# Kernel tuning notes

Measured on AMD Instinct MI355X. Metric: run time of the kernel, lower is better.

The kernel has to match this reference:

```python
import jax, jax.numpy as jnp
import numpy as np

N_HEADS = 4
TAU = 0.1

def _ln(x, w, b):
    m = jnp.mean(x, axis=-1, keepdims=True)
    v = jnp.mean(jnp.square(x - m), axis=-1, keepdims=True)
    return (x - m) / jnp.sqrt(v + 1e-6) * w + b

def _l2norm(x):
    # torch F.normalize(dim=1): x / max(||x||_2, 1e-12)
    n = jnp.linalg.norm(x, axis=1, keepdims=True)
    return x / jnp.maximum(n, 1e-12)

def _sincos_pe(T, dim):
    pos = jnp.arange(T, dtype=jnp.float32)[:, None]
    div = jnp.exp(jnp.arange(0, dim, 2, dtype=jnp.float32) * (-np.log(10000.0) / dim))
    ang = pos * div[None, :]
    # interleave: even indices sin, odd indices cos
    return jnp.stack([jnp.sin(ang), jnp.cos(ang)], axis=-1).reshape(T, dim)

def reference(x, p1_w, p1_b, pln1_w, pln1_b, p2_w, pln2_w, pln2_b,
              in_proj_w, in_proj_b, out_proj_w, out_proj_b,
              ln1_w, ln1_b, lin1_w, lin1_b, lin2_w, lin2_b, ln2_w, ln2_b, head_w):
    B, T, D = x.shape
    E = p2_w.shape[0]           # bottleneck_dim = 256
    H = N_HEADS
    hd = E // H
    # projector: Linear -> LN -> GELU -> Linear(no bias) -> LN
    h = jax.nn.gelu(_ln(x.reshape(B * T, D) @ p1_w.T + p1_b, pln1_w, pln1_b), approximate=False)
    h = _ln(h @ p2_w.T, pln2_w, pln2_b).reshape(B, T, E)
    h = h + _sincos_pe(T, E)[None]
    causal = jnp.tril(jnp.ones((T, T), dtype=bool))
    L = in_proj_w.shape[0]
    for i in range(L):  # post-norm TransformerEncoderLayer
        qkv = h @ in_proj_w[i].T + in_proj_b[i]        # [B,T,3E]
        q, k, v = jnp.split(qkv, 3, axis=-1)
        q = q.reshape(B, T, H, hd).transpose(0, 2, 1, 3)
        k = k.reshape(B, T, H, hd).transpose(0, 2, 1, 3)
        v = v.reshape(B, T, H, hd).transpose(0, 2, 1, 3)
        scores = jnp.einsum('bhtd,bhsd->bhts', q, k) / np.float32(np.sqrt(hd))
        scores = jnp.where(causal[None, None], scores, -jnp.inf)
        probs = jax.nn.softmax(scores, axis=-1)        # materialized attn probs (eager path)
        attn = jnp.einsum('bhts,bhsd->bhtd', probs, v).transpose(0, 2, 1, 3).reshape(B, T, E)
        attn = attn @ out_proj_w[i].T + out_proj_b[i]
        h = _ln(h + attn, ln1_w[i], ln1_b[i])
        ff = jax.nn.gelu(h @ lin1_w[i].T + lin1_b[i], approximate=False) @ lin2_w[i].T + lin2_b[i]
        h = _ln(h + ff, ln2_w[i], ln2_b[i])
    flat = _l2norm(h.reshape(B * T, E))
    wn = _l2norm(head_w)
    return (flat @ wn.T / TAU).reshape(B, T, -1)

def setup_inputs() -> dict:
    key = jax.random.key(0)
    ks = jax.random.split(key, 8)
    B, T, D, E, HID, CLS, L = 2048, 20, 2048, 256, 1024, 1000, 2
    s = 0.02
    def w(k, shape):
        return jax.random.normal(k, shape, jnp.float32) * s
    return {
        'x': jax.random.normal(ks[0], (B, T, D), jnp.float32),
        'p1_w': w(ks[1], (HID, D)), 'p1_b': jnp.zeros((HID,), jnp.float32),
        'pln1_w': jnp.ones((HID,), jnp.float32), 'pln1_b': jnp.zeros((HID,), jnp.float32),
        'p2_w': w(ks[2], (E, HID)),
        'pln2_w': jnp.ones((E,), jnp.float32), 'pln2_b': jnp.zeros((E,), jnp.float32),
        'in_proj_w': w(ks[3], (L, 3 * E, E)), 'in_proj_b': jnp.zeros((L, 3 * E), jnp.float32),
        'out_proj_w': w(ks[4], (L, E, E)), 'out_proj_b': jnp.zeros((L, E), jnp.float32),
        'ln1_w': jnp.ones((L, E), jnp.float32), 'ln1_b': jnp.zeros((L, E), jnp.float32),
        'lin1_w': w(ks[5], (L, 4 * E, E)), 'lin1_b': jnp.zeros((L, 4 * E), jnp.float32),
        'lin2_w': w(ks[6], (L, E, 4 * E)), 'lin2_b': jnp.zeros((L, E), jnp.float32),
        'ln2_w': jnp.ones((L, E), jnp.float32), 'ln2_b': jnp.zeros((L, E), jnp.float32),
        'head_w': w(ks[7], (CLS, E)),
    }
```

## Files before the change

### kernel.cpp

```cpp
#include <hip/hip_runtime.h>
#include <math.h>

#define CDIV(a,b) (((a)+(b)-1)/(b))

typedef unsigned short bfu;
typedef short   s16x8 __attribute__((ext_vector_type(8)));
typedef float   f32x4 __attribute__((ext_vector_type(4)));

#define GLOAD16(gp, lp) __builtin_amdgcn_global_load_lds( \
    (const __attribute__((address_space(1))) void*)(gp),  \
    (__attribute__((address_space(3))) void*)(lp), 16, 0, 0)

static __device__ __forceinline__ float gelu_exact(float x) {
    return 0.5f * x * (1.0f + erff(x * 0.7071067811865475f));
}
static __device__ __forceinline__ bfu f2bf(float x) {
    unsigned int u = __float_as_uint(x);
    unsigned int r = u + 0x7fffu + ((u >> 16) & 1u);
    return (bfu)(r >> 16);
}
static __device__ __forceinline__ float bf2f(bfu b) {
    return __uint_as_float(((unsigned int)b) << 16);
}
static __device__ __forceinline__ float wave_sum(float v) {
    #pragma unroll
    for (int off = 32; off; off >>= 1) v += __shfl_xor(v, off, 64);
    return v;
}

__global__ __launch_bounds__(256)
void cvt_kernel(const float* __restrict__ in, bfu* __restrict__ out, int n4)
{
    int i = blockIdx.x * 256 + threadIdx.x;
    const int stride = gridDim.x * 256;
    for (; i < n4; i += stride) {
        float4 f = ((const float4*)in)[i];
        ushort4 o;
        o.x = f2bf(f.x); o.y = f2bf(f.y); o.z = f2bf(f.z); o.w = f2bf(f.w);
        ((ushort4*)out)[i] = o;
    }
}

__global__ __launch_bounds__(256)
void cvt6_kernel(const float* __restrict__ s0, const float* __restrict__ s1,
                 const float* __restrict__ s2, const float* __restrict__ s3,
                 const float* __restrict__ s4, const float* __restrict__ s5,
                 bfu* __restrict__ dst)
{
    const int c0 = 524288;
    const int c1 = c0 + 65536;
    const int c2 = c1 + 98304;
    const int c3 = c2 + 32768;
    const int c4 = c3 + 131072;
    const int c5 = c4 + 131072;
    int i = blockIdx.x * 256 + threadIdx.x;
    const int stride = gridDim.x * 256;
    for (; i < c5; i += stride) {
        const float* s; int base;
        if      (i < c0) { s = s0; base = 0;  }
        else if (i < c1) { s = s1; base = c0; }
        else if (i < c2) { s = s2; base = c1; }
        else if (i < c3) { s = s3; base = c2; }
        else if (i < c4) { s = s4; base = c3; }
        else             { s = s5; base = c4; }
        float4 f = ((const float4*)s)[i - base];
        ushort4 o;
        o.x = f2bf(f.x); o.y = f2bf(f.y); o.z = f2bf(f.z); o.w = f2bf(f.w);
        ((ushort4*)dst)[i] = o;
    }
}

__global__ __launch_bounds__(256)
void pe_kernel(float* __restrict__ pe)
{
    const int t = blockIdx.x;
    const int c = threadIdx.x;
    const float div = expf((float)(c & ~1) * (-9.210340371976184f / 256.0f));
    const float ang = (float)t * div;
    pe[t * 256 + c] = (c & 1) ? cosf(ang) : sinf(ang);
}

template<bool GELU_EP, bool OUT_BF16>
__global__ __launch_bounds__(512, 4)
void mfma_gemmA(const bfu* __restrict__ A, const bfu* __restrict__ W,
                const float* __restrict__ bias, void* __restrict__ Cv,
                int M, int N, int K, float scale, int ntx)
{
    __shared__ bfu ldsA[3][4096];
    __shared__ bfu ldsW[3][8192];

    const int tid  = threadIdx.x;
    const int lane = tid & 63;
    const int wv   = tid >> 6;
    const int nwg  = gridDim.x;
    const int lid  = (nwg & 7) ? (int)blockIdx.x
                               : ((int)blockIdx.x & 7) * (nwg >> 3) + ((int)blockIdx.x >> 3);
    const int row0 = (lid / ntx) * 128;
    const int col0 = (lid % ntx) * 256;

    const int srow = wv * 16 + (lane >> 2);
    const int sk   = ((lane & 3) ^ ((lane >> 2) & 3) ^ (lane >> 4)) * 8;
    const bfu* aS  = A + (size_t)(row0 + srow) * K + sk;
    const bfu* wS0 = W + (size_t)(col0 + srow)        * K + sk;
    const bfu* wS1 = W + (size_t)(col0 + srow + 128)  * K + sk;
    const int dOff = wv * 512;

    const int wr = wv >> 2, wc = wv & 3;
    const int fr = lane & 15;
    const int g4 = lane >> 4;
    const int slot = ((g4 ^ (fr & 3) ^ ((fr >> 2) & 3))) * 8;

    f32x4 acc[4][4];
    #pragma unroll
    for (int i = 0; i < 4; ++i)
        #pragma unroll
        for (int j = 0; j < 4; ++j) acc[i][j] = (f32x4)0.f;

    const int nt = K >> 5;

#define STAGEA_(b_, t_) do { \
    const size_t ko_ = (size_t)(t_) * 32; \
    GLOAD16(aS  + ko_, &ldsA[b_][dOff]); \
    GLOAD16(wS0 + ko_, &ldsW[b_][dOff]); \
    GLOAD16(wS1 + ko_, &ldsW[b_][4096 + dOff]); \
} while (0)

    STAGEA_(0, 0);
    STAGEA_(1, 1);

    int cur = 0, nxt2 = 2;
    for (int t = 0; t < nt; ++t) {
        if (t + 1 < nt) asm volatile("s_waitcnt vmcnt(3)" ::: "memory");
        else            asm volatile("s_waitcnt vmcnt(0)" ::: "memory");
        asm volatile("s_barrier" ::: "memory");

        if (t + 2 < nt) STAGEA_(nxt2, t + 2);

        const bfu* Ab = ldsA[cur];
        const bfu* Wb = ldsW[cur];

        s16x8 bfr[4], afr[4];
        #pragma unroll
        for (int j = 0; j < 4; ++j)
            bfr[j] = *(const s16x8*)&Wb[(wc * 64 + j * 16 + fr) * 32 + slot];
        #pragma unroll
        for (int i = 0; i < 4; ++i)
            afr[i] = *(const s16x8*)&Ab[(wr * 64 + i * 16 + fr) * 32 + slot];

        __builtin_amdgcn_s_setprio(1);
        #pragma unroll
        for (int i = 0; i < 4; ++i)
            #pragma unroll
            for (int j = 0; j < 4; ++j)
                acc[i][j] = __builtin_amdgcn_mfma_f32_16x16x32_bf16(afr[i], bfr[j], acc[i][j], 0, 0, 0);
        __builtin_amdgcn_s_setprio(0);

        cur  = (cur  == 2) ? 0 : cur  + 1;
        nxt2 = (nxt2 == 2) ? 0 : nxt2 + 1;
    }
#undef STAGEA_

    #pragma unroll
    for (int i = 0; i < 4; ++i) {
        const int r = row0 + wr * 64 + 16 * i + g4 * 4;
        #pragma unroll
        for (int j = 0; j < 4; ++j) {
            const int c = col0 + wc * 64 + 16 * j + fr;
            if (c < N) {
                const float bsum = bias ? bias[c] : 0.f;
                #pragma unroll
                for (int rr = 0; rr < 4; ++rr) {
                    float v = acc[i][j][rr] + bsum;
                    if (GELU_EP) v = gelu_exact(v);
                    v *= scale;
                    if (OUT_BF16) ((bfu*)Cv)[(size_t)(r + rr) * N + c] = f2bf(v);
                    else          ((float*)Cv)[(size_t)(r + rr) * N + c] = v;
                }
            }
        }
    }
}

template<bool RES, bool ADD_PE, bool L2N>
__global__ __launch_bounds__(512, 2)
void mfma_gemm_ln(const bfu* __restrict__ A, const bfu* __restrict__ W,
                  const float* __restrict__ bias, const float* __restrict__ R,
                  const float* __restrict__ lnw, const float* __restrict__ lnb,
                  const float* __restrict__ pe, float* __restrict__ Yf,
                  bfu* __restrict__ Yb, int M, int K, int T)
{
    __shared__ bfu ldsA[3][4096];
    __shared__ bfu ldsW[3][8192];

    const int tid  = threadIdx.x;
    const int lane = tid & 63;
    const int wv   = tid >> 6;
    const int nwg  = gridDim.x;
    const int lid  = (nwg & 7) ? (int)blockIdx.x
                               : ((int)blockIdx.x & 7) * (nwg >> 3) + ((int)blockIdx.x >> 3);
    const int row0 = lid * 128;

    const int srow = wv * 16 + (lane >> 2);
    const int sk   = ((lane & 3) ^ ((lane >> 2) & 3) ^ (lane >> 4)) * 8;
    const bfu* aS  = A + (size_t)(row0 + srow) * K + sk;
    const bfu* wS0 = W + (size_t)(srow)        * K + sk;
    const bfu* wS1 = W + (size_t)(srow + 128)  * K + sk;
    const int dOff = wv * 512;

    const int wr = wv >> 2, wc = wv & 3;
    const int fr = lane & 15;
    const int g4 = lane >> 4;
    const int slot = ((g4 ^ (fr & 3) ^ ((fr >> 2) & 3))) * 8;

    f32x4 acc[4][4];
    #pragma unroll
    for (int i = 0; i < 4; ++i)
        #pragma unroll
        for (int j = 0; j < 4; ++j) acc[i][j] = (f32x4)0.f;

    const int nt = K >> 5;

#define STAGELN(b_, t_) do { \
    const size_t ko_ = (size_t)(t_) * 32; \
    GLOAD16(aS  + ko_, &ldsA[b_][dOff]); \
    GLOAD16(wS0 + ko_, &ldsW[b_][dOff]); \
    GLOAD16(wS1 + ko_, &ldsW[b_][4096 + dOff]); \
} while (0)

    STAGELN(0, 0);
    STAGELN(1, 1);

    int cur = 0, nxt2 = 2;
    for (int t = 0; t < nt; ++t) {
        if (t + 1 < nt) asm volatile("s_waitcnt vmcnt(3)" ::: "memory");
        else            asm volatile("s_waitcnt vmcnt(0)" ::: "memory");
        asm volatile("s_barrier" ::: "memory");

        if (t + 2 < nt) STAGELN(nxt2, t + 2);

        const bfu* Ab = ldsA[cur];
        const bfu* Wb = ldsW[cur];

        s16x8 bfr[4], afr[4];
        #pragma unroll
        for (int j = 0; j < 4; ++j)
            bfr[j] = *(const s16x8*)&Wb[(wc * 64 + j * 16 + fr) * 32 + slot];
        #pragma unroll
        for (int i = 0; i < 4; ++i)
            afr[i] = *(const s16x8*)&Ab[(wr * 64 + i * 16 + fr) * 32 + slot];

        __builtin_amdgcn_s_setprio(1);
        #pragma unroll
        for (int i = 0; i < 4; ++i)
            #pragma unroll
            for (int j = 0; j < 4; ++j)
                acc[i][j] = __builtin_amdgcn_mfma_f32_16x16x32_bf16(afr[i], bfr[j], acc[i][j], 0, 0, 0);
        __builtin_amdgcn_s_setprio(0);

        cur  = (cur  == 2) ? 0 : cur  + 1;
        nxt2 = (nxt2 == 2) ? 0 : nxt2 + 1;
    }
#undef STAGELN

    __syncthreads();

    float* red   = (float*)ldsA;
    float* stats = red + 1024;

    float bj[4];
    #pragma unroll
    for (int j = 0; j < 4; ++j)
        bj[j] = bias ? bias[wc * 64 + j * 16 + fr] : 0.f;

    #pragma unroll
    for (int i = 0; i < 4; ++i) {
        #pragma unroll
        for (int rr = 0; rr < 4; ++rr) {
            const int rl = wr * 64 + i * 16 + g4 * 4 + rr;
            const size_t r = (size_t)(row0 + rl);
            float s = 0.f, q = 0.f;
            #pragma unroll
            for (int j = 0; j < 4; ++j) {
                float v = acc[i][j][rr] + bj[j];
                if (RES) v += R[r * 256 + (wc * 64 + j * 16 + fr)];
                acc[i][j][rr] = v;
                s += v; q += v * v;
            }
            #pragma unroll
            for (int off = 1; off < 16; off <<= 1) {
                s += __shfl_xor(s, off, 64);
                q += __shfl_xor(q, off, 64);
            }
            if (fr == 0) { red[rl * 4 + wc] = s; red[512 + rl * 4 + wc] = q; }
        }
    }
    __syncthreads();
    if (tid < 128) {
        const float s = red[tid*4+0] + red[tid*4+1] + red[tid*4+2] + red[tid*4+3];
        const float q = red[512+tid*4+0] + red[512+tid*4+1] + red[512+tid*4+2] + red[512+tid*4+3];
        const float mean = s * (1.f / 256.f);
        const float var  = q * (1.f / 256.f) - mean * mean;
        stats[tid]       = mean;
        stats[128 + tid] = rsqrtf(var + 1e-6f);
    }
    __syncthreads();

    float lw[4], lb[4];
    #pragma unroll
    for (int j = 0; j < 4; ++j) {
        const int c = wc * 64 + j * 16 + fr;
        lw[j] = lnw[c]; lb[j] = lnb[c];
    }
    #pragma unroll
    for (int i = 0; i < 4; ++i) {
        #pragma unroll
        for (int rr = 0; rr < 4; ++rr) {
            const int rl = wr * 64 + i * 16 + g4 * 4 + rr;
            const size_t r = (size_t)(row0 + rl);
            const float mean = stats[rl], rstd = stats[128 + rl];
            const int tmod = (int)(r % (size_t)T);
            float ysq = 0.f;
            #pragma unroll
            for (int j = 0; j < 4; ++j) {
                const int c = wc * 64 + j * 16 + fr;
                float y = (acc[i][j][rr] - mean) * rstd * lw[j] + lb[j];
                if (ADD_PE) y += pe[tmod * 256 + c];
                if (!L2N) {
                    Yf[r * 256 + c] = y;
                    Yb[r * 256 + c] = f2bf(y);
                } else {
                    acc[i][j][rr] = y;
                    ysq += y * y;
                }
            }
            if (L2N) {
                #pragma unroll
                for (int off = 1; off < 16; off <<= 1) ysq += __shfl_xor(ysq, off, 64);
                if (fr == 0) red[rl * 4 + wc] = ysq;
            }
        }
    }
    if (L2N) {
        __syncthreads();
        if (tid < 128) {
            const float n = sqrtf(red[tid*4+0] + red[tid*4+1] + red[tid*4+2] + red[tid*4+3]);
            stats[tid] = 1.f / fmaxf(n, 1e-12f);
        }
        __syncthreads();
        #pragma unroll
        for (int i = 0; i < 4; ++i) {
            #pragma unroll
            for (int rr = 0; rr < 4; ++rr) {
                const int rl = wr * 64 + i * 16 + g4 * 4 + rr;
                const size_t r = (size_t)(row0 + rl);
                const float rn = stats[rl];
                #pragma unroll
                for (int j = 0; j < 4; ++j) {
                    const int c = wc * 64 + j * 16 + fr;
                    Yb[r * 256 + c] = f2bf(acc[i][j][rr] * rn);
                }
            }
        }
    }
}

__global__ __launch_bounds__(256)
void ln1024_kernel(const bfu* __restrict__ X, const float* __restrict__ w,
                   const float* __restrict__ b, bfu* __restrict__ Y)
{
    __shared__ float sbuf[4];
    const int row = blockIdx.x;
    const bfu* xr = X + (size_t)row * 1024;

    ushort4 t4 = *(const ushort4*)(xr + threadIdx.x * 4);
    float v[4] = {bf2f(t4.x), bf2f(t4.y), bf2f(t4.z), bf2f(t4.w)};

    float s = v[0] + v[1] + v[2] + v[3];
    s = wave_sum(s);
    const int lane = threadIdx.x & 63, wid = threadIdx.x >> 6;
    if (lane == 0) sbuf[wid] = s;
    __syncthreads();
    const float mean = (sbuf[0] + sbuf[1] + sbuf[2] + sbuf[3]) * (1.f / 1024.f);

    float q = 0.f;
    #pragma unroll
    for (int j = 0; j < 4; ++j) { float d = v[j] - mean; q += d * d; }
    q = wave_sum(q);
    __syncthreads();
    if (lane == 0) sbuf[wid] = q;
    __syncthreads();
    const float var  = (sbuf[0] + sbuf[1] + sbuf[2] + sbuf[3]) * (1.f / 1024.f);
    const float rstd = rsqrtf(var + 1e-6f);

    ushort4 o;
    #pragma unroll
    for (int j = 0; j < 4; ++j) {
        const int c = threadIdx.x * 4 + j;
        float y = gelu_exact((v[j] - mean) * rstd * w[c] + b[c]);
        ((bfu*)&o)[j] = f2bf(y);
    }
    *(ushort4*)(Y + (size_t)row * 1024 + threadIdx.x * 4) = o;
}

__global__ __launch_bounds__(64)
void attn_kernel(const bfu* __restrict__ qkv, bfu* __restrict__ out,
                 int B, int T, int H)
{
    __shared__ float qs[20][65];
    __shared__ float ks[20][65];
    __shared__ float vs[20][65];
    __shared__ float probs[64];

    const int blk = blockIdx.x;
    const int b = blk / H;
    const int h = blk % H;
    const int tid = threadIdx.x;

    const bfu* base0 = qkv + (size_t)(b * T) * 768 + h * 64;
    #pragma unroll
    for (int m = 0; m < 3; ++m) {
        const bfu* src = base0 + m * 256;
        float (*dst)[65] = (m == 0) ? qs : (m == 1) ? ks : vs;
        #pragma unroll
        for (int i = 0; i < 5; ++i) {
            const int idx = i * 64 + tid;
            const int t = idx >> 4, s = (idx & 15) * 4;
            ushort4 u = *(const ushort4*)(src + (size_t)t * 768 + s);
            dst[t][s+0] = bf2f(u.x); dst[t][s+1] = bf2f(u.y);
            dst[t][s+2] = bf2f(u.z); dst[t][s+3] = bf2f(u.w);
        }
    }
    __syncthreads();

    for (int t = 0; t < T; ++t) {
        float sc = -INFINITY;
        if (tid <= t) {
            float s = 0.f;
            #pragma unroll
            for (int d = 0; d < 64; ++d) s = fmaf(qs[t][d], ks[tid][d], s);
            sc = s * 0.125f;
        }
        float m = sc;
        #pragma unroll
        for (int off = 32; off; off >>= 1) m = fmaxf(m, __shfl_xor(m, off, 64));
        float p = (tid <= t) ? expf(sc - m) : 0.f;
        float sum = p;
        #pragma unroll
        for (int off = 32; off; off >>= 1) sum += __shfl_xor(sum, off, 64);
        p /= sum;
        probs[tid] = p;
        __syncthreads();

        float o = 0.f;
        for (int s = 0; s <= t; ++s) o = fmaf(probs[s], vs[s][tid], o);
        out[(size_t)(b * T + t) * 256 + h * 64 + tid] = f2bf(o);
        __syncthreads();
    }
}

__global__ __launch_bounds__(256)
void l2norm_kernel(const float* __restrict__ X, bfu* __restrict__ Y)
{
    const int row  = blockIdx.x * 4 + (threadIdx.x >> 6);
    const int lane = threadIdx.x & 63;
    float4 v = *(const float4*)(X + (size_t)row * 256 + lane * 4);
    float n = sqrtf(wave_sum(v.x*v.x + v.y*v.y + v.z*v.z + v.w*v.w));
    n = 1.f / fmaxf(n, 1e-12f);
    ushort4 o = {f2bf(v.x*n), f2bf(v.y*n), f2bf(v.z*n), f2bf(v.w*n)};
    *(ushort4*)(Y + (size_t)row * 256 + lane * 4) = o;
}

extern "C" void kernel_launch(void* const* d_in, const int* in_sizes, int n_in,
                              void* d_out, int out_size, void* d_ws, size_t ws_size,
                              hipStream_t stream)
{
    const float* x         = (const float*)d_in[0];
    const float* p1_w      = (const float*)d_in[1];
    const float* p1_b      = (const float*)d_in[2];
    const float* pln1_w    = (const float*)d_in[3];
    const float* pln1_b    = (const float*)d_in[4];
    const float* p2_w      = (const float*)d_in[5];
    const float* pln2_w    = (const float*)d_in[6];
    const float* pln2_b    = (const float*)d_in[7];
    const float* in_proj_w = (const float*)d_in[8];
    const float* in_proj_b = (const float*)d_in[9];
    const float* out_proj_w= (const float*)d_in[10];
    const float* out_proj_b= (const float*)d_in[11];
    const float* ln1_w     = (const float*)d_in[12];
    const float* ln1_b     = (const float*)d_in[13];
    const float* lin1_w    = (const float*)d_in[14];
    const float* lin1_b    = (const float*)d_in[15];
    const float* lin2_w    = (const float*)d_in[16];
    const float* lin2_b    = (const float*)d_in[17];
    const float* ln2_w     = (const float*)d_in[18];
    const float* ln2_b     = (const float*)d_in[19];
    const float* head_w    = (const float*)d_in[20];

    const int B = 2048, T = 20, E = 256, HID = 1024, CLS = 1000, L = 2, H = 4;
    const int M = B * T;
    const int D = 2048;

    char* p = (char*)d_ws;
    bfu*   xb     = (bfu*)p;    p += (size_t)M * D * 2;
    bfu*   h1b    = (bfu*)p;    p += (size_t)M * HID * 2;
    bfu*   wblk   = (bfu*)p;    p += (size_t)3932160 * 2;
    bfu*   wnb    = (bfu*)p;    p += (size_t)1024 * E * 2;
    float* pe     = (float*)p;  p += (size_t)T * 256 * 4;

    char* q = (char*)xb;
    float* h      = (float*)q;  q += (size_t)M * E * 4;
    bfu*   hb     = (bfu*)q;    q += (size_t)M * E * 2;
    bfu*   abf    = (bfu*)q;    q += (size_t)M * E * 2;

    bfu* p1wb  = wblk;
    bfu* p2wb  = p1wb  + (size_t)HID * D;
    bfu* qkvwb = p2wb  + (size_t)E * HID;
    bfu* outwb = qkvwb + (size_t)L * 3 * E * E;
    bfu* l1wb  = outwb + (size_t)L * E * E;
    bfu* l2wb  = l1wb  + (size_t)L * 4 * E * E;

    float* out   = (float*)d_out;
    bfu*   qkvb  = (bfu*)d_out;

    cvt_kernel<<<2048, 256, 0, stream>>>(x, xb, M * D / 4);
    cvt6_kernel<<<2048, 256, 0, stream>>>(p1_w, p2_w, in_proj_w, out_proj_w, lin1_w, lin2_w, wblk);
    pe_kernel<<<T, 256, 0, stream>>>(pe);

    mfma_gemmA<false, true><<<dim3((M/128) * (HID/256)), 512, 0, stream>>>(
        xb, p1wb, p1_b, h1b, M, HID, D, 1.f, HID/256);
    ln1024_kernel<<<M, 256, 0, stream>>>(h1b, pln1_w, pln1_b, h1b);
    mfma_gemm_ln<false, true, false><<<dim3(M/128), 512, 0, stream>>>(
        h1b, p2wb, nullptr, nullptr, pln2_w, pln2_b, pe, h, hb, M, HID, T);

    for (int l = 0; l < L; ++l) {
        mfma_gemmA<false, true><<<dim3((M/128) * 3), 512, 0, stream>>>(
            hb, qkvwb + (size_t)l * 3*E*E, in_proj_b + (size_t)l * 3*E, qkvb, M, 3*E, E, 1.f, 3);
        attn_kernel<<<B * H, 64, 0, stream>>>(qkvb, abf, B, T, H);
        mfma_gemm_ln<true, false, false><<<dim3(M/128), 512, 0, stream>>>(
            abf, outwb + (size_t)l * E*E, out_proj_b + (size_t)l * E, h,
            ln1_w + (size_t)l * E, ln1_b + (size_t)l * E, nullptr, h, hb, M, E, T);
        mfma_gemmA<true, true><<<dim3((M/128) * 4), 512, 0, stream>>>(
            hb, l1wb + (size_t)l * 4*E*E, lin1_b + (size_t)l * 4*E, h1b, M, HID, E, 1.f, 4);
        if (l < L - 1) {
            mfma_gemm_ln<true, false, false><<<dim3(M/128), 512, 0, stream>>>(
                h1b, l2wb + (size_t)l * E*4*E, lin2_b + (size_t)l * E, h,
                ln2_w + (size_t)l * E, ln2_b + (size_t)l * E, nullptr, h, hb, M, HID, T);
        } else {
            mfma_gemm_ln<true, false, true><<<dim3(M/128), 512, 0, stream>>>(
                h1b, l2wb + (size_t)l * E*4*E, lin2_b + (size_t)l * E, h,
                ln2_w + (size_t)l * E, ln2_b + (size_t)l * E, nullptr, nullptr, hb, M, HID, T);
        }
    }

    l2norm_kernel<<<CLS/4, 256, 0, stream>>>(head_w, wnb);
    mfma_gemmA<false, false><<<dim3((M/128) * 4), 512, 0, stream>>>(
        hb, wnb, nullptr, out, M, CLS, E, 10.f, 4);
}
```

Baseline: 1.184 ms.

## Add 256x256-tile ping-pong MFMA GEMM for the first projector layer

Adds a new bf16 MFMA GEMM kernel with 256x256 output tiles, a double-buffered LDS pipeline split into two K-halves, and interleaved barriers with s_setprio around MFMA bursts. It replaces the 128x256-tile kernel for the large x @ p1_w GEMM (K=2048). The goal is more reuse per LDS load and better overlap of global loads with MFMA work. In exchange it uses more registers and LDS per block, which lowers occupancy to two blocks per CU and halves the grid size.

```diff
diff --git a/kernel.cpp b/kernel.cpp
--- a/kernel.cpp
+++ b/kernel.cpp
@@ -78,6 +78,145 @@
     const float div = expf((float)(c & ~1) * (-9.210340371976184f / 256.0f));
     const float ang = (float)t * div;
     pe[t * 256 + c] = (c & 1) ? cosf(ang) : sinf(ang);
+}
+
+template<bool OUT_BF16>
+__global__ __launch_bounds__(512, 2)
+void mfma_gemm8p(const bfu* __restrict__ A, const bfu* __restrict__ W,
+                 const float* __restrict__ bias, void* __restrict__ Cv,
+                 int M, int N, int K, float scale, int ntx)
+{
+    __shared__ bfu ldsA[2][2][8192];
+    __shared__ bfu ldsB[2][2][8192];
+
+    const int tid  = threadIdx.x;
+    const int lane = tid & 63;
+    const int wv   = tid >> 6;
+    const int nwg  = gridDim.x;
+    const int lid  = (nwg & 7) ? (int)blockIdx.x
+                               : ((int)blockIdx.x & 7) * (nwg >> 3) + ((int)blockIdx.x >> 3);
+    const int row0 = (lid / ntx) * 256;
+    const int col0 = (lid % ntx) * 256;
+
+    const int srow = wv * 16 + (lane >> 2);
+    const int sk   = ((lane & 3) ^ ((lane >> 2) & 3) ^ (lane >> 4)) * 8;
+    const bfu* aR0 = A + (size_t)(row0 + srow)       * K + sk;
+    const bfu* aR1 = A + (size_t)(row0 + 128 + srow) * K + sk;
+    const bfu* wR0 = W + (size_t)(col0 + srow)       * K + sk;
+    const bfu* wR1 = W + (size_t)(col0 + 128 + srow) * K + sk;
+    const int dOff = wv * 512;
+
+    const int wr = wv >> 2, wc = wv & 3;
+    const int fr = lane & 15;
+    const int g4 = lane >> 4;
+    const int slot = ((g4 ^ (fr & 3) ^ ((fr >> 2) & 3))) * 8;
+
+    f32x4 acc[8][4];
+    #pragma unroll
+    for (int i = 0; i < 8; ++i)
+        #pragma unroll
+        for (int j = 0; j < 4; ++j) acc[i][j] = (f32x4)0.f;
+
+    const int nt = K >> 6;
+
+#define STG8(t_, kh_) do { \
+    const size_t ko_ = (size_t)(t_) * 64 + (size_t)(kh_) * 32; \
+    const int b_ = (t_) & 1; \
+    GLOAD16(aR0 + ko_, &ldsA[b_][kh_][dOff]); \
+    GLOAD16(aR1 + ko_, &ldsA[b_][kh_][4096 + dOff]); \
+    GLOAD16(wR0 + ko_, &ldsB[b_][kh_][dOff]); \
+    GLOAD16(wR1 + ko_, &ldsB[b_][kh_][4096 + dOff]); \
+} while (0)
+
+    STG8(0, 0); STG8(0, 1); STG8(1, 0); STG8(1, 1);
+
+    for (int t = 0; t < nt; ++t) {
+        const int buf = t & 1;
+        if (t + 1 < nt) asm volatile("s_waitcnt vmcnt(8)" ::: "memory");
+        else            asm volatile("s_waitcnt vmcnt(0)" ::: "memory");
+        __builtin_amdgcn_s_barrier();
+
+        const bfu* Ab0 = ldsA[buf][0];
+        const bfu* Bb0 = ldsB[buf][0];
+        const bfu* Ab1 = ldsA[buf][1];
+        const bfu* Bb1 = ldsB[buf][1];
+
+        s16x8 a[8], b[4];
+        #pragma unroll
+        for (int mi = 0; mi < 8; ++mi)
+            a[mi] = *(const s16x8*)&Ab0[(wr * 128 + mi * 16 + fr) * 32 + slot];
+        b[0] = *(const s16x8*)&Bb0[(wc * 64 +  0 + fr) * 32 + slot];
+        b[1] = *(const s16x8*)&Bb0[(wc * 64 + 16 + fr) * 32 + slot];
+        __builtin_amdgcn_s_barrier();
+        __builtin_amdgcn_s_setprio(1);
+        #pragma unroll
+        for (int mi = 0; mi < 8; ++mi) {
+            acc[mi][0] = __builtin_amdgcn_mfma_f32_16x16x32_bf16(a[mi], b[0], acc[mi][0], 0, 0, 0);
+            acc[mi][1] = __builtin_amdgcn_mfma_f32_16x16x32_bf16(a[mi], b[1], acc[mi][1], 0, 0, 0);
+        }
+        __builtin_amdgcn_s_setprio(0);
+        __builtin_amdgcn_s_barrier();
+
+        b[2] = *(const s16x8*)&Bb0[(wc * 64 + 32 + fr) * 32 + slot];
+        b[3] = *(const s16x8*)&Bb0[(wc * 64 + 48 + fr) * 32 + slot];
+        __builtin_amdgcn_s_barrier();
+        __builtin_amdgcn_s_setprio(1);
+        #pragma unroll
+        for (int mi = 0; mi < 8; ++mi) {
+            acc[mi][2] = __builtin_amdgcn_mfma_f32_16x16x32_bf16(a[mi], b[2], acc[mi][2], 0, 0, 0);
+            acc[mi][3] = __builtin_amdgcn_mfma_f32_16x16x32_bf16(a[mi], b[3], acc[mi][3], 0, 0, 0);
+        }
+        __builtin_amdgcn_s_setprio(0);
+        __builtin_amdgcn_s_barrier();
+        if (t + 2 < nt) STG8(t + 2, 0);
+
+        #pragma unroll
+        for (int mi = 0; mi < 8; ++mi)
+            a[mi] = *(const s16x8*)&Ab1[(wr * 128 + mi * 16 + fr) * 32 + slot];
+        b[0] = *(const s16x8*)&Bb1[(wc * 64 +  0 + fr) * 32 + slot];
+        b[1] = *(const s16x8*)&Bb1[(wc * 64 + 16 + fr) * 32 + slot];
+        __builtin_amdgcn_s_barrier();
+        __builtin_amdgcn_s_setprio(1);
+        #pragma unroll
+        for (int mi = 0; mi < 8; ++mi) {
+            acc[mi][0] = __builtin_amdgcn_mfma_f32_16x16x32_bf16(a[mi], b[0], acc[mi][0], 0, 0, 0);
+            acc[mi][1] = __builtin_amdgcn_mfma_f32_16x16x32_bf16(a[mi], b[1], acc[mi][1], 0, 0, 0);
+        }
+        __builtin_amdgcn_s_setprio(0);
+        __builtin_amdgcn_s_barrier();
+
+        b[2] = *(const s16x8*)&Bb1[(wc * 64 + 32 + fr) * 32 + slot];
+        b[3] = *(const s16x8*)&Bb1[(wc * 64 + 48 + fr) * 32 + slot];
+        __builtin_amdgcn_s_barrier();
+        __builtin_amdgcn_s_setprio(1);
+        #pragma unroll
+        for (int mi = 0; mi < 8; ++mi) {
+            acc[mi][2] = __builtin_amdgcn_mfma_f32_16x16x32_bf16(a[mi], b[2], acc[mi][2], 0, 0, 0);
+            acc[mi][3] = __builtin_amdgcn_mfma_f32_16x16x32_bf16(a[mi], b[3], acc[mi][3], 0, 0, 0);
+        }
+        __builtin_amdgcn_s_setprio(0);
+        __builtin_amdgcn_s_barrier();
+        if (t + 2 < nt) STG8(t + 2, 1);
+    }
+#undef STG8
+
+    #pragma unroll
+    for (int i = 0; i < 8; ++i) {
+        const int r = row0 + wr * 128 + 16 * i + g4 * 4;
+        #pragma unroll
+        for (int j = 0; j < 4; ++j) {
+            const int c = col0 + wc * 64 + 16 * j + fr;
+            if (c < N) {
+                const float bsum = bias ? bias[c] : 0.f;
+                #pragma unroll
+                for (int rr = 0; rr < 4; ++rr) {
+                    float v = (acc[i][j][rr] + bsum) * scale;
+                    if (OUT_BF16) ((bfu*)Cv)[(size_t)(r + rr) * N + c] = f2bf(v);
+                    else          ((float*)Cv)[(size_t)(r + rr) * N + c] = v;
+                }
+            }
+        }
+    }
 }
 
 template<bool GELU_EP, bool OUT_BF16>
@@ -526,7 +665,7 @@
     cvt6_kernel<<<2048, 256, 0, stream>>>(p1_w, p2_w, in_proj_w, out_proj_w, lin1_w, lin2_w, wblk);
     pe_kernel<<<T, 256, 0, stream>>>(pe);
 
-    mfma_gemmA<false, true><<<dim3((M/128) * (HID/256)), 512, 0, stream>>>(
+    mfma_gemm8p<true><<<dim3((M/256) * (HID/256)), 512, 0, stream>>>(
         xb, p1wb, p1_b, h1b, M, HID, D, 1.f, HID/256);
     ln1024_kernel<<<M, 256, 0, stream>>>(h1b, pln1_w, pln1_b, h1b);
     mfma_gemm_ln<false, true, false><<<dim3(M/128), 512, 0, stream>>>(
```

After: 1.212 ms. 2.4% more time.

## Fuse fp32-to-bf16 input conversion into first projector GEMM; use shuffles in attention

Applied to the files above, without the earlier changes.

Removes the standalone conversion kernel that turned the large fp32 input into bf16. A new GEMM variant loads fp32 A tiles straight from global memory into registers, converts them to bf16 and writes them to LDS, while weights still stream in through global_load_lds. This avoids writing and re-reading a large bf16 copy of x, at the cost of twice the A-tile read bytes inside the GEMM and extra conversion ALU work per tile, with up to four column-tile blocks each re-reading and re-converting the same rows. The attention kernel also broadcasts probabilities with wave shuffles instead of LDS plus two barriers per timestep.

```diff
diff --git a/kernel.cpp b/kernel.cpp
--- a/kernel.cpp
+++ b/kernel.cpp
@@ -26,19 +26,6 @@
     #pragma unroll
     for (int off = 32; off; off >>= 1) v += __shfl_xor(v, off, 64);
     return v;
-}
-
-__global__ __launch_bounds__(256)
-void cvt_kernel(const float* __restrict__ in, bfu* __restrict__ out, int n4)
-{
-    int i = blockIdx.x * 256 + threadIdx.x;
-    const int stride = gridDim.x * 256;
-    for (; i < n4; i += stride) {
-        float4 f = ((const float4*)in)[i];
-        ushort4 o;
-        o.x = f2bf(f.x); o.y = f2bf(f.y); o.z = f2bf(f.z); o.w = f2bf(f.w);
-        ((ushort4*)out)[i] = o;
-    }
 }
 
 __global__ __launch_bounds__(256)
@@ -80,6 +67,126 @@
     pe[t * 256 + c] = (c & 1) ? cosf(ang) : sinf(ang);
 }
 
+template<bool OUT_BF16>
+__global__ __launch_bounds__(512, 4)
+void mfma_gemmX(const float* __restrict__ Af, const bfu* __restrict__ W,
+                const float* __restrict__ bias, void* __restrict__ Cv,
+                int M, int N, int K, int ntx)
+{
+    __shared__ bfu ldsA[3][4096];
+    __shared__ bfu ldsW[3][8192];
+
+    const int tid  = threadIdx.x;
+    const int lane = tid & 63;
+    const int wv   = tid >> 6;
+    const int nwg  = gridDim.x;
+    const int lid  = (nwg & 7) ? (int)blockIdx.x
+                               : ((int)blockIdx.x & 7) * (nwg >> 3) + ((int)blockIdx.x >> 3);
+    const int row0 = (lid / ntx) * 128;
+    const int col0 = (lid % ntx) * 256;
+
+    const int arow = tid >> 2;
+    const int aq   = tid & 3;
+    const int agq  = aq ^ (arow & 3) ^ ((arow >> 2) & 3);
+    const float* aP = Af + (size_t)(row0 + arow) * K + agq * 8;
+
+    const int srow = wv * 16 + (lane >> 2);
+    const int sk   = ((lane & 3) ^ ((lane >> 2) & 3) ^ (lane >> 4)) * 8;
+    const bfu* wS0 = W + (size_t)(col0 + srow)        * K + sk;
+    const bfu* wS1 = W + (size_t)(col0 + srow + 128)  * K + sk;
+    const int dOff = wv * 512;
+
+    const int wr = wv >> 2, wc = wv & 3;
+    const int fr = lane & 15;
+    const int g4 = lane >> 4;
+    const int slot = ((g4 ^ (fr & 3) ^ ((fr >> 2) & 3))) * 8;
+
+    f32x4 acc[4][4];
+    #pragma unroll
+    for (int i = 0; i < 4; ++i)
+        #pragma unroll
+        for (int j = 0; j < 4; ++j) acc[i][j] = (f32x4)0.f;
+
+    const int nt = K >> 5;
+    float4 pa0[2], pa1[2];
+
+#define ALOAD(t_, s_) do { \
+    const float* p_ = aP + (size_t)(t_) * 32; \
+    pa0[s_] = *(const float4*)(p_); \
+    pa1[s_] = *(const float4*)(p_ + 4); \
+} while (0)
+#define WSTAGE(t_) do { \
+    const size_t ko_ = (size_t)(t_) * 32; \
+    GLOAD16(wS0 + ko_, &ldsW[(t_) % 3][dOff]); \
+    GLOAD16(wS1 + ko_, &ldsW[(t_) % 3][4096 + dOff]); \
+} while (0)
+#define AWRITE(t_, s_) do { \
+    s16x8 r_; \
+    r_[0]=(short)f2bf(pa0[s_].x); r_[1]=(short)f2bf(pa0[s_].y); \
+    r_[2]=(short)f2bf(pa0[s_].z); r_[3]=(short)f2bf(pa0[s_].w); \
+    r_[4]=(short)f2bf(pa1[s_].x); r_[5]=(short)f2bf(pa1[s_].y); \
+    r_[6]=(short)f2bf(pa1[s_].z); r_[7]=(short)f2bf(pa1[s_].w); \
+    *(s16x8*)&ldsA[(t_) % 3][arow * 32 + aq * 8] = r_; \
+} while (0)
+
+    ALOAD(0, 0); WSTAGE(0);
+    ALOAD(1, 1); WSTAGE(1);
+    AWRITE(0, 0);
+    asm volatile("s_waitcnt vmcnt(4) lgkmcnt(0)" ::: "memory");
+    asm volatile("s_barrier" ::: "memory");
+
+    for (int t = 0; t < nt; ++t) {
+        if (t + 2 < nt) { ALOAD(t + 2, t & 1); WSTAGE(t + 2); }
+
+        const bfu* Ab = ldsA[t % 3];
+        const bfu* Wb = ldsW[t % 3];
+
+        s16x8 bfr[4], afr[4];
+        #pragma unroll
+        for (int j = 0; j < 4; ++j)
+            bfr[j] = *(const s16x8*)&Wb[(wc * 64 + j * 16 + fr) * 32 + slot];
+        #pragma unroll
+        for (int i = 0; i < 4; ++i)
+            afr[i] = *(const s16x8*)&Ab[(wr * 64 + i * 16 + fr) * 32 + slot];
+
+        __builtin_amdgcn_s_setprio(1);
+        #pragma unroll
+        for (int i = 0; i < 4; ++i)
+            #pragma unroll
+            for (int j = 0; j < 4; ++j)
+                acc[i][j] = __builtin_amdgcn_mfma_f32_16x16x32_bf16(afr[i], bfr[j], acc[i][j], 0, 0, 0);
+        __builtin_amdgcn_s_setprio(0);
+
+        if (t + 1 < nt) {
+            AWRITE(t + 1, (t + 1) & 1);
+            if (t + 2 < nt) asm volatile("s_waitcnt vmcnt(4) lgkmcnt(0)" ::: "memory");
+            else            asm volatile("s_waitcnt vmcnt(0) lgkmcnt(0)" ::: "memory");
+            asm volatile("s_barrier" ::: "memory");
+        }
+    }
+#undef ALOAD
+#undef WSTAGE
+#undef AWRITE
+
+    #pragma unroll
+    for (int i = 0; i < 4; ++i) {
+        const int r = row0 + wr * 64 + 16 * i + g4 * 4;
+        #pragma unroll
+        for (int j = 0; j < 4; ++j) {
+            const int c = col0 + wc * 64 + 16 * j + fr;
+            if (c < N) {
+                const float bsum = bias ? bias[c] : 0.f;
+                #pragma unroll
+                for (int rr = 0; rr < 4; ++rr) {
+                    float v = acc[i][j][rr] + bsum;
+                    if (OUT_BF16) ((bfu*)Cv)[(size_t)(r + rr) * N + c] = f2bf(v);
+                    else          ((float*)Cv)[(size_t)(r + rr) * N + c] = v;
+                }
+            }
+        }
+    }
+}
+
 template<bool GELU_EP, bool OUT_BF16>
 __global__ __launch_bounds__(512, 4)
 void mfma_gemmA(const bfu* __restrict__ A, const bfu* __restrict__ W,
@@ -409,7 +516,6 @@
     __shared__ float qs[20][65];
     __shared__ float ks[20][65];
     __shared__ float vs[20][65];
-    __shared__ float probs[64];
 
     const int blk = blockIdx.x;
     const int b = blk / H;
@@ -448,13 +554,10 @@
         #pragma unroll
         for (int off = 32; off; off >>= 1) sum += __shfl_xor(sum, off, 64);
         p /= sum;
-        probs[tid] = p;
-        __syncthreads();
 
         float o = 0.f;
-        for (int s = 0; s <= t; ++s) o = fmaf(probs[s], vs[s][tid], o);
+        for (int s = 0; s <= t; ++s) o = fmaf(__shfl(p, s, 64), vs[s][tid], o);
         out[(size_t)(b * T + t) * 256 + h * 64 + tid] = f2bf(o);
-        __syncthreads();
     }
 }
 
@@ -501,16 +604,13 @@
     const int D = 2048;
 
     char* p = (char*)d_ws;
-    bfu*   xb     = (bfu*)p;    p += (size_t)M * D * 2;
     bfu*   h1b    = (bfu*)p;    p += (size_t)M * HID * 2;
     bfu*   wblk   = (bfu*)p;    p += (size_t)3932160 * 2;
     bfu*   wnb    = (bfu*)p;    p += (size_t)1024 * E * 2;
     float* pe     = (float*)p;  p += (size_t)T * 256 * 4;
-
-    char* q = (char*)xb;
-    float* h      = (float*)q;  q += (size_t)M * E * 4;
-    bfu*   hb     = (bfu*)q;    q += (size_t)M * E * 2;
-    bfu*   abf    = (bfu*)q;    q += (size_t)M * E * 2;
+    float* h      = (float*)p;  p += (size_t)M * E * 4;
+    bfu*   hb     = (bfu*)p;    p += (size_t)M * E * 2;
+    bfu*   abf    = (bfu*)p;    p += (size_t)M * E * 2;
 
     bfu* p1wb  = wblk;
     bfu* p2wb  = p1wb  + (size_t)HID * D;
@@ -522,12 +622,11 @@
     float* out   = (float*)d_out;
     bfu*   qkvb  = (bfu*)d_out;
 
-    cvt_kernel<<<2048, 256, 0, stream>>>(x, xb, M * D / 4);
     cvt6_kernel<<<2048, 256, 0, stream>>>(p1_w, p2_w, in_proj_w, out_proj_w, lin1_w, lin2_w, wblk);
     pe_kernel<<<T, 256, 0, stream>>>(pe);
 
-    mfma_gemmA<false, true><<<dim3((M/128) * (HID/256)), 512, 0, stream>>>(
-        xb, p1wb, p1_b, h1b, M, HID, D, 1.f, HID/256);
+    mfma_gemmX<true><<<dim3((M/128) * (HID/256)), 512, 0, stream>>>(
+        x, p1wb, p1_b, h1b, M, HID, D, HID/256);
     ln1024_kernel<<<M, 256, 0, stream>>>(h1b, pln1_w, pln1_b, h1b);
     mfma_gemm_ln<false, true, false><<<dim3(M/128), 512, 0, stream>>>(
         h1b, p2wb, nullptr, nullptr, pln2_w, pln2_b, pe, h, hb, M, HID, T);
```

After: 1.554 ms. 31.3% more time.
